# Optimization experiments

Hardware: AMD Instinct MI355X
Metric: run time of the kernel (lower is better)

## Reference

```python
import jax, jax.numpy as jnp
import numpy as np

N_HEADS = 16
D_K = 64  # d_model / n_heads = 1024 / 16


def setup_inputs() -> dict:
    key = jax.random.key(0)
    ks = jax.random.split(key, 7)
    B, S, D = 4, 2048, 1024
    scale = 1.0 / np.sqrt(D)
    return {
        "Q": jax.random.normal(ks[0], (B, S, D), dtype=jnp.float32),
        "K": jax.random.normal(ks[1], (B, S, D), dtype=jnp.float32),
        "V": jax.random.normal(ks[2], (B, S, D), dtype=jnp.float32),
        # Linear weights stored as [in, out] so y = x @ W (bias=False in original).
        "WQ": jax.random.normal(ks[3], (D, D), dtype=jnp.float32) * scale,
        "WK": jax.random.normal(ks[4], (D, D), dtype=jnp.float32) * scale,
        "WV": jax.random.normal(ks[5], (D, D), dtype=jnp.float32) * scale,
        "Wfc": jax.random.normal(ks[6], (D, D), dtype=jnp.float32) * scale,
    }


def reference(Q, K, V, WQ, WK, WV, Wfc):
    B = Q.shape[0]
    # NOTE: the original uses a raw reshape [B, S, H*dk] -> [B, H, S, dk]
    # (NOT the usual view+transpose); row-major reshape reproduces it exactly.
    q = (Q @ WQ).reshape(B, N_HEADS, -1, D_K)  # [B, H, S, dk]
    k = (K @ WK).reshape(B, N_HEADS, -1, D_K)
    v = (V @ WV).reshape(B, N_HEADS, -1, D_K)
    scores = jnp.einsum("bhqd,bhkd->bhqk", q, k) / jnp.sqrt(jnp.asarray(D_K, q.dtype))
    attn = jax.nn.softmax(scores, axis=-1)
    ctx = jnp.einsum("bhqk,bhkd->bhqd", attn, v)  # [B, H, S, dk]
    ctx = jnp.transpose(ctx, (0, 2, 1, 3)).reshape(B, -1, N_HEADS * D_K)  # [B, S, D]
    return ctx @ Wfc
```

## Files before the change

kernel.cpp:

```cpp
#include <hip/hip_runtime.h>
#include <stdint.h>
#include <math.h>


typedef __attribute__((ext_vector_type(8))) short short8;
typedef __attribute__((ext_vector_type(4))) float f32x4;
typedef __attribute__((ext_vector_type(16))) float f32x16;
typedef __attribute__((ext_vector_type(2))) unsigned int u32x2;
typedef __attribute__((ext_vector_type(4))) unsigned int u32x4;
typedef __attribute__((ext_vector_type(8))) _Float16 half8;

__device__ __forceinline__ unsigned short bf16rne(float f) {
  unsigned int u = __builtin_bit_cast(unsigned int, f);
  unsigned int r = u + 0x7FFFu + ((u >> 16) & 1u);
  return (unsigned short)(r >> 16);
}

__device__ __forceinline__ void gld_lds16(const void* g, void* l) {
  typedef __attribute__((address_space(3))) unsigned int lds_u32;
  typedef const __attribute__((address_space(1))) unsigned int glb_u32;
  __builtin_amdgcn_global_load_lds((glb_u32*)(uintptr_t)g,
                                   (lds_u32*)(unsigned int)(uintptr_t)l,
                                   16, 0, 0);
}

__device__ __forceinline__ unsigned pkrtz(float a, float b) {
  auto h = __builtin_amdgcn_cvt_pkrtz(a, b);
  return __builtin_bit_cast(unsigned, h);
}

__global__ void convert_x_kernel(const float* __restrict__ Q,
                                 const float* __restrict__ K,
                                 const float* __restrict__ V,
                                 unsigned short* __restrict__ Xb) {
  const int z = blockIdx.y;
  const float* src = (z == 0) ? Q : (z == 1) ? K : V;
  const size_t i0 = ((size_t)blockIdx.x * 256 + threadIdx.x) * 8;
  const f32x4 a = *(const f32x4*)(src + i0);
  const f32x4 c = *(const f32x4*)(src + i0 + 4);
  u32x4 o;
  o[0] = (unsigned)bf16rne(a[0]) | ((unsigned)bf16rne(a[1]) << 16);
  o[1] = (unsigned)bf16rne(a[2]) | ((unsigned)bf16rne(a[3]) << 16);
  o[2] = (unsigned)bf16rne(c[0]) | ((unsigned)bf16rne(c[1]) << 16);
  o[3] = (unsigned)bf16rne(c[2]) | ((unsigned)bf16rne(c[3]) << 16);
  *(u32x4*)(Xb + (size_t)z * 8388608 + i0) = o;
}

__global__ void convert_w_kernel(const float* __restrict__ W0,
                                 const float* __restrict__ W1,
                                 const float* __restrict__ W2,
                                 const float* __restrict__ W3,
                                 unsigned short* __restrict__ Wt) {
  const int z = blockIdx.z;
  const float* W = (z == 0) ? W0 : (z == 1) ? W1 : (z == 2) ? W2 : W3;
  unsigned short* dst = Wt + (size_t)z * 1048576;
  __shared__ float tile[32][33];
  const int tx = threadIdx.x & 31, ty = threadIdx.x >> 5;
  const int k0 = blockIdx.x * 32, n0 = blockIdx.y * 32;
#pragma unroll
  for (int yy = 0; yy < 32; yy += 8)
    tile[ty + yy][tx] = W[(size_t)(k0 + ty + yy) * 1024 + n0 + tx];
  __syncthreads();
#pragma unroll
  for (int yy = 0; yy < 32; yy += 8)
    dst[(size_t)(n0 + ty + yy) * 1024 + k0 + tx] = bf16rne(tile[tx][ty + yy]);
}

__global__ __launch_bounds__(256, 2) void gemm_bt_kernel(
    const unsigned short* __restrict__ A, const unsigned short* __restrict__ Bt,
    unsigned short* __restrict__ Cbf, float* __restrict__ Cf32, float scaleZ0) {
  constexpr int K = 1024, N = 1024;
  const int z = blockIdx.z;
  const unsigned short* Ab = A + (size_t)z * 8192 * 1024;
  const unsigned short* Bb = Bt + (size_t)z * 1024 * 1024;
  const int tid = threadIdx.x;
  const int lane = tid & 63;
  const int w = tid >> 6;
  const int l15 = lane & 15, quad = lane >> 4;
  const int rowBase = blockIdx.x * 128;
  const int colBase = blockIdx.y * 128;
  const int wrow = (w >> 1) * 64;
  const int wcol = (w & 1) * 64;
  __shared__ __align__(16) unsigned short As[128 * 32];
  __shared__ __align__(16) unsigned short Bs[128 * 32];

  const f32x4 z4 = {0.0f, 0.0f, 0.0f, 0.0f};
  f32x4 acc[4][4];
#pragma unroll
  for (int i = 0; i < 4; i++)
#pragma unroll
    for (int j = 0; j < 4; j++) acc[i][j] = z4;

  const int s0 = tid, s1 = tid + 256;
  const int rA0 = s0 >> 2, cA0 = (s0 & 3) * 8;
  const int rA1 = s1 >> 2, cA1 = (s1 & 3) * 8;

  for (int k0 = 0; k0 < K; k0 += 32) {
    gld_lds16(Ab + (size_t)(rowBase + rA0) * K + k0 + cA0, (void*)(As + s0 * 8));
    gld_lds16(Ab + (size_t)(rowBase + rA1) * K + k0 + cA1, (void*)(As + s1 * 8));
    gld_lds16(Bb + (size_t)(colBase + rA0) * K + k0 + cA0, (void*)(Bs + s0 * 8));
    gld_lds16(Bb + (size_t)(colBase + rA1) * K + k0 + cA1, (void*)(Bs + s1 * 8));
    __syncthreads();
    short8 af[4], bfr[4];
#pragma unroll
    for (int i = 0; i < 4; i++)
      af[i] = *(const short8*)(As + (wrow + i * 16 + l15) * 32 + quad * 8);
#pragma unroll
    for (int j = 0; j < 4; j++)
      bfr[j] = *(const short8*)(Bs + (wcol + j * 16 + l15) * 32 + quad * 8);
#pragma unroll
    for (int i = 0; i < 4; i++)
#pragma unroll
      for (int j = 0; j < 4; j++)
        acc[i][j] =
            __builtin_amdgcn_mfma_f32_16x16x32_bf16(af[i], bfr[j], acc[i][j], 0, 0, 0);
    __syncthreads();
  }

  const float sc = (z == 0) ? scaleZ0 : 1.0f;
#pragma unroll
  for (int i = 0; i < 4; i++) {
#pragma unroll
    for (int j = 0; j < 4; j++) {
#pragma unroll
      for (int r = 0; r < 4; r++) {
        const int row = rowBase + wrow + i * 16 + quad * 4 + r;
        const int col = colBase + wcol + j * 16 + l15;
        const float v = acc[i][j][r] * sc;
        if (Cbf != nullptr) {
          Cbf[(size_t)z * 8192 * 1024 + (size_t)row * N + col] = bf16rne(v);
        } else {
          Cf32[(size_t)row * N + col] = v;
        }
      }
    }
  }
}

__global__ void vtrans_kernel(const unsigned short* __restrict__ linv,
                              unsigned short* __restrict__ Vt) {
  const int st = blockIdx.x, bh = blockIdx.y;
  const unsigned short* vp = linv + (size_t)bh * 131072;
  __shared__ unsigned short tile[64 * 136];
  const int tid = threadIdx.x;
#pragma unroll
  for (int it = 0; it < 4; it++) {
    const int idx = it * 256 + tid;
    const int s = idx >> 3, d0 = (idx & 7) * 8;
    const u32x4 vv = *(const u32x4*)(vp + (size_t)(st * 128 + s) * 64 + d0);
#pragma unroll
    for (int m = 0; m < 4; m++) {
      const unsigned lo = vv[m] & 0xffffu, hi = vv[m] >> 16;
      const float f0 = __builtin_bit_cast(float, lo << 16);
      const float f1 = __builtin_bit_cast(float, hi << 16);
      const _Float16 h0 = (_Float16)f0, h1 = (_Float16)f1;
      tile[(d0 + 2 * m) * 136 + s] = __builtin_bit_cast(unsigned short, h0);
      tile[(d0 + 2 * m + 1) * 136 + s] = __builtin_bit_cast(unsigned short, h1);
    }
  }
  __syncthreads();
#pragma unroll
  for (int it = 0; it < 4; it++) {
    const int idx = it * 256 + tid;
    const int d = idx >> 4, s0 = (idx & 15) * 8;
    const u32x4 o = *(const u32x4*)(tile + d * 136 + s0);
    *(u32x4*)(Vt + (size_t)bh * 131072 + (size_t)d * 2048 + st * 128 + s0) = o;
  }
}

__global__ __launch_bounds__(256, 3) void attn_kernel(
    const unsigned short* __restrict__ lin, const _Float16* __restrict__ Vt,
    unsigned short* __restrict__ ctxr) {
  const int bh = blockIdx.x;
  const int qt = blockIdx.y;
  const int b = bh >> 4, h = bh & 15;
  const int tid = threadIdx.x, lane = tid & 63, w = tid >> 6;
  const int l31 = lane & 31, hl = lane >> 5, x7 = l31 & 7;
  const size_t headOff = (size_t)(b * 2048 + h * 128) * 1024;
  const unsigned short* qp = lin + headOff;
  const unsigned short* kp = lin + 8388608 + headOff;
  const _Float16* vtp = Vt + (size_t)bh * 131072;

  __shared__ __align__(16) unsigned short smem[24576];
  unsigned short(*Ks)[4096] = (unsigned short(*)[4096])smem;
  _Float16(*Vs)[4096] = (_Float16(*)[4096])(smem + 8192);
  _Float16* Pl = (_Float16*)(smem + 16384) + w * 2048;

  const int stageV = (w >= 2);
  const int wbase = (stageV ? (w - 2) : w) * 256 + lane;
  auto stage = [&](int bufn, int key0) {
#pragma unroll
    for (int i = 0; i < 4; i++) {
      const int slot = wbase + i * 64;
      const int row = slot >> 3;
      const int seg = (slot & 7) ^ (row & 7);
      if (!stageV) {
        gld_lds16(kp + (size_t)(key0 + row) * 64 + seg * 8,
                  (void*)(&Ks[bufn][slot * 8]));
      } else {
        gld_lds16(vtp + (size_t)row * 2048 + key0 + seg * 8,
                  (void*)(&Vs[bufn][slot * 8]));
      }
    }
  };

  const int qrow0 = qt * 128 + w * 32;
  short8 bq[4];
#pragma unroll
  for (int ks = 0; ks < 4; ks++)
    bq[ks] = *(const short8*)(qp + (size_t)(qrow0 + l31) * 64 + ks * 16 + hl * 8);

  f32x16 z16;
#pragma unroll
  for (int r = 0; r < 16; r++) z16[r] = 0.0f;
  f32x16 co[2] = {z16, z16};
  float mrun = -INFINITY, lrun = 0.0f;

  stage(0, 0);
  __syncthreads();

  for (int kt = 0; kt < 32; kt++) {
    const int cur = kt & 1;
    if (kt < 31) stage(cur ^ 1, (kt + 1) * 64);

    f32x16 sacc[2] = {z16, z16};
    __builtin_amdgcn_s_setprio(1);
#pragma unroll
    for (int g = 0; g < 2; g++) {
#pragma unroll
      for (int ks = 0; ks < 4; ks++) {
        const int slot = (g * 32 + l31) * 8 + ((2 * ks + hl) ^ x7);
        const short8 kf = *(const short8*)(&Ks[cur][slot * 8]);
        sacc[g] =
            __builtin_amdgcn_mfma_f32_32x32x16_bf16(kf, bq[ks], sacc[g], 0, 0, 0);
      }
    }
    __builtin_amdgcn_s_setprio(0);

    half8 vf[2][2][2];
#pragma unroll
    for (int dt = 0; dt < 2; dt++)
#pragma unroll
      for (int g = 0; g < 2; g++)
#pragma unroll
        for (int s = 0; s < 2; s++) {
          const int slot = (dt * 32 + l31) * 8 + ((4 * g + 2 * s + hl) ^ x7);
          vf[dt][g][s] = *(const half8*)(&Vs[cur][slot * 8]);
        }

    float pmax;
    {
      float tm[8];
#pragma unroll
      for (int r = 0; r < 8; r++)
        tm[r] = fmaxf(fmaxf(sacc[0][r], sacc[0][r + 8]),
                      fmaxf(sacc[1][r], sacc[1][r + 8]));
      const float a0 = fmaxf(fmaxf(tm[0], tm[1]), fmaxf(tm[2], tm[3]));
      const float a1 = fmaxf(fmaxf(tm[4], tm[5]), fmaxf(tm[6], tm[7]));
      pmax = fmaxf(a0, a1);
    }
    pmax = fmaxf(pmax, __shfl_xor(pmax, 32, 64));
    if (!__all(pmax - mrun <= 8.0f)) {
      const float mnew = fmaxf(mrun, pmax);
      const float a = exp2f(mrun - mnew);
      mrun = mnew;
      lrun *= a;
#pragma unroll
      for (int r = 0; r < 16; r++) {
        co[0][r] *= a;
        co[1][r] *= a;
      }
    }
    float ls0 = 0.0f, ls1 = 0.0f, ls2 = 0.0f, ls3 = 0.0f;
#pragma unroll
    for (int g = 0; g < 2; g++) {
#pragma unroll
      for (int r = 0; r < 16; r += 4) {
        const float p0 = exp2f(sacc[g][r + 0] - mrun);
        const float p1 = exp2f(sacc[g][r + 1] - mrun);
        const float p2 = exp2f(sacc[g][r + 2] - mrun);
        const float p3 = exp2f(sacc[g][r + 3] - mrun);
        sacc[g][r + 0] = p0;
        sacc[g][r + 1] = p1;
        sacc[g][r + 2] = p2;
        sacc[g][r + 3] = p3;
        ls0 += p0;
        ls1 += p1;
        ls2 += p2;
        ls3 += p3;
      }
    }
    lrun += (ls0 + ls1) + (ls2 + ls3);

#pragma unroll
    for (int g = 0; g < 2; g++) {
#pragma unroll
      for (int rg = 0; rg < 4; rg++) {
        u32x2 pw;
        pw[0] = pkrtz(sacc[g][4 * rg + 0], sacc[g][4 * rg + 1]);
        pw[1] = pkrtz(sacc[g][4 * rg + 2], sacc[g][4 * rg + 3]);
        *(u32x2*)(Pl + l31 * 64 + (((4 * g + rg) ^ x7) * 8) + hl * 4) = pw;
      }
      half8 pf[2];
#pragma unroll
      for (int s = 0; s < 2; s++)
        pf[s] =
            *(const half8*)(Pl + l31 * 64 + (((4 * g + 2 * s + hl) ^ x7) * 8));
      __builtin_amdgcn_s_setprio(1);
#pragma unroll
      for (int dt = 0; dt < 2; dt++)
#pragma unroll
        for (int s = 0; s < 2; s++)
          co[dt] = __builtin_amdgcn_mfma_f32_32x32x16_f16(vf[dt][g][s], pf[s],
                                                          co[dt], 0, 0, 0);
      __builtin_amdgcn_s_setprio(0);
    }
    __syncthreads();
  }

  lrun += __shfl_xor(lrun, 32, 64);
  const float inv = 1.0f / lrun;
  unsigned short* Cw = smem + w * 2304;
#pragma unroll
  for (int dt = 0; dt < 2; dt++) {
#pragma unroll
    for (int r = 0; r < 16; r++) {
      const int d = dt * 32 + (r & 3) + 8 * (r >> 2) + 4 * hl;
      Cw[l31 * 72 + d] = bf16rne(co[dt][r] * inv);
    }
  }
  __syncthreads();
#pragma unroll
  for (int it = 0; it < 4; it++) {
    const int q = it * 8 + (lane >> 3);
    const int seg = lane & 7;
    const u32x4 o = *(const u32x4*)(Cw + q * 72 + seg * 8);
    *(u32x4*)(ctxr + (size_t)(b * 2048 + qrow0 + q) * 1024 + h * 64 + seg * 8) = o;
  }
}

extern "C" void kernel_launch(void* const* d_in, const int* in_sizes, int n_in,
                              void* d_out, int out_size, void* d_ws, size_t ws_size,
                              hipStream_t stream) {
  const float* Q = (const float*)d_in[0];
  const float* K = (const float*)d_in[1];
  const float* V = (const float*)d_in[2];
  const float* WQ = (const float*)d_in[3];
  const float* WK = (const float*)d_in[4];
  const float* WV = (const float*)d_in[5];
  const float* Wfc = (const float*)d_in[6];
  float* out = (float*)d_out;

  unsigned short* ws = (unsigned short*)d_ws;
  unsigned short* Xb = ws;
  unsigned short* ctxr = ws;
  unsigned short* Vt = ws + 8388608;
  unsigned short* Wt = ws + 25165824;
  unsigned short* lin = ws + 29360128;

  convert_x_kernel<<<dim3(4096, 3), 256, 0, stream>>>(Q, K, V, Xb);
  convert_w_kernel<<<dim3(32, 32, 4), 256, 0, stream>>>(WQ, WK, WV, Wfc, Wt);
  const float qscale = 0.125f * 1.4426950408889634f;
  gemm_bt_kernel<<<dim3(64, 8, 3), 256, 0, stream>>>(Xb, Wt, lin, nullptr, qscale);
  vtrans_kernel<<<dim3(16, 64), 256, 0, stream>>>(lin + 16777216, Vt);
  attn_kernel<<<dim3(64, 16), 256, 0, stream>>>(lin, (const _Float16*)Vt, ctxr);
  gemm_bt_kernel<<<dim3(64, 8, 1), 256, 0, stream>>>(ctxr, Wt + 3 * 1048576, nullptr,
                                                     out, 1.0f);
}
```

Baseline: 422.5 us.

## Process two 32-row query groups per wave in attention to reuse K/V tiles

Each wave now handles 64 query rows (two groups of 32) instead of 32, so each block covers 256 queries and the grid's query dimension is halved. K and V fragments loaded from LDS are reused across both query groups, and the global-to-LDS staging of each K/V tile is amortized over twice as many queries. The cost is more registers per thread (doubled accumulators and softmax state), so launch bounds drop from 3 to 2 blocks per CU. The grid also shrinks to 512 blocks, which lowers parallelism.

```diff
diff --git a/kernel.cpp b/kernel.cpp
--- a/kernel.cpp
+++ b/kernel.cpp
@@ -168,7 +168,7 @@
   }
 }
 
-__global__ __launch_bounds__(256, 3) void attn_kernel(
+__global__ __launch_bounds__(256, 2) void attn_kernel(
     const unsigned short* __restrict__ lin, const _Float16* __restrict__ Vt,
     unsigned short* __restrict__ ctxr) {
   const int bh = blockIdx.x;
@@ -204,17 +204,22 @@
     }
   };
 
-  const int qrow0 = qt * 128 + w * 32;
-  short8 bq[4];
-#pragma unroll
-  for (int ks = 0; ks < 4; ks++)
-    bq[ks] = *(const short8*)(qp + (size_t)(qrow0 + l31) * 64 + ks * 16 + hl * 8);
+  const int qrow0 = qt * 256 + w * 64;
+  short8 bq[2][4];
+#pragma unroll
+  for (int qg = 0; qg < 2; qg++)
+#pragma unroll
+    for (int ks = 0; ks < 4; ks++)
+      bq[qg][ks] = *(const short8*)(qp +
+                                    (size_t)(qrow0 + qg * 32 + l31) * 64 +
+                                    ks * 16 + hl * 8);
 
   f32x16 z16;
 #pragma unroll
   for (int r = 0; r < 16; r++) z16[r] = 0.0f;
-  f32x16 co[2] = {z16, z16};
-  float mrun = -INFINITY, lrun = 0.0f;
+  f32x16 co[2][2] = {{z16, z16}, {z16, z16}};
+  float mrun[2] = {-INFINITY, -INFINITY};
+  float lrun[2] = {0.0f, 0.0f};
 
   stage(0, 0);
   __syncthreads();
@@ -223,18 +228,25 @@
     const int cur = kt & 1;
     if (kt < 31) stage(cur ^ 1, (kt + 1) * 64);
 
-    f32x16 sacc[2] = {z16, z16};
-    __builtin_amdgcn_s_setprio(1);
-#pragma unroll
-    for (int g = 0; g < 2; g++) {
+    short8 kf[2][4];
+#pragma unroll
+    for (int g = 0; g < 2; g++)
 #pragma unroll
       for (int ks = 0; ks < 4; ks++) {
         const int slot = (g * 32 + l31) * 8 + ((2 * ks + hl) ^ x7);
-        const short8 kf = *(const short8*)(&Ks[cur][slot * 8]);
-        sacc[g] =
-            __builtin_amdgcn_mfma_f32_32x32x16_bf16(kf, bq[ks], sacc[g], 0, 0, 0);
-      }
-    }
+        kf[g][ks] = *(const short8*)(&Ks[cur][slot * 8]);
+      }
+
+    f32x16 sacc[2][2] = {{z16, z16}, {z16, z16}};
+    __builtin_amdgcn_s_setprio(1);
+#pragma unroll
+    for (int qg = 0; qg < 2; qg++)
+#pragma unroll
+      for (int g = 0; g < 2; g++)
+#pragma unroll
+        for (int ks = 0; ks < 4; ks++)
+          sacc[qg][g] = __builtin_amdgcn_mfma_f32_32x32x16_bf16(
+              kf[g][ks], bq[qg][ks], sacc[qg][g], 0, 0, 0);
     __builtin_amdgcn_s_setprio(0);
 
     half8 vf[2][2][2];
@@ -248,90 +260,96 @@
           vf[dt][g][s] = *(const half8*)(&Vs[cur][slot * 8]);
         }
 
-    float pmax;
-    {
-      float tm[8];
-#pragma unroll
-      for (int r = 0; r < 8; r++)
-        tm[r] = fmaxf(fmaxf(sacc[0][r], sacc[0][r + 8]),
-                      fmaxf(sacc[1][r], sacc[1][r + 8]));
-      const float a0 = fmaxf(fmaxf(tm[0], tm[1]), fmaxf(tm[2], tm[3]));
-      const float a1 = fmaxf(fmaxf(tm[4], tm[5]), fmaxf(tm[6], tm[7]));
-      pmax = fmaxf(a0, a1);
-    }
-    pmax = fmaxf(pmax, __shfl_xor(pmax, 32, 64));
-    if (!__all(pmax - mrun <= 8.0f)) {
-      const float mnew = fmaxf(mrun, pmax);
-      const float a = exp2f(mrun - mnew);
-      mrun = mnew;
-      lrun *= a;
+#pragma unroll
+    for (int qg = 0; qg < 2; qg++) {
+      float pmax;
+      {
+        float tm[8];
+#pragma unroll
+        for (int r = 0; r < 8; r++)
+          tm[r] = fmaxf(fmaxf(sacc[qg][0][r], sacc[qg][0][r + 8]),
+                        fmaxf(sacc[qg][1][r], sacc[qg][1][r + 8]));
+        const float a0 = fmaxf(fmaxf(tm[0], tm[1]), fmaxf(tm[2], tm[3]));
+        const float a1 = fmaxf(fmaxf(tm[4], tm[5]), fmaxf(tm[6], tm[7]));
+        pmax = fmaxf(a0, a1);
+      }
+      pmax = fmaxf(pmax, __shfl_xor(pmax, 32, 64));
+      if (!__all(pmax - mrun[qg] <= 8.0f)) {
+        const float mnew = fmaxf(mrun[qg], pmax);
+        const float a = exp2f(mrun[qg] - mnew);
+        mrun[qg] = mnew;
+        lrun[qg] *= a;
+#pragma unroll
+        for (int r = 0; r < 16; r++) {
+          co[qg][0][r] *= a;
+          co[qg][1][r] *= a;
+        }
+      }
+      float ls0 = 0.0f, ls1 = 0.0f, ls2 = 0.0f, ls3 = 0.0f;
+#pragma unroll
+      for (int g = 0; g < 2; g++) {
+#pragma unroll
+        for (int r = 0; r < 16; r += 4) {
+          const float p0 = exp2f(sacc[qg][g][r + 0] - mrun[qg]);
+          const float p1 = exp2f(sacc[qg][g][r + 1] - mrun[qg]);
+          const float p2 = exp2f(sacc[qg][g][r + 2] - mrun[qg]);
+          const float p3 = exp2f(sacc[qg][g][r + 3] - mrun[qg]);
+          sacc[qg][g][r + 0] = p0;
+          sacc[qg][g][r + 1] = p1;
+          sacc[qg][g][r + 2] = p2;
+          sacc[qg][g][r + 3] = p3;
+          ls0 += p0;
+          ls1 += p1;
+          ls2 += p2;
+          ls3 += p3;
+        }
+      }
+      lrun[qg] += (ls0 + ls1) + (ls2 + ls3);
+
+#pragma unroll
+      for (int g = 0; g < 2; g++) {
+#pragma unroll
+        for (int rg = 0; rg < 4; rg++) {
+          u32x2 pw;
+          pw[0] = pkrtz(sacc[qg][g][4 * rg + 0], sacc[qg][g][4 * rg + 1]);
+          pw[1] = pkrtz(sacc[qg][g][4 * rg + 2], sacc[qg][g][4 * rg + 3]);
+          *(u32x2*)(Pl + l31 * 64 + (((4 * g + rg) ^ x7) * 8) + hl * 4) = pw;
+        }
+        half8 pf[2];
+#pragma unroll
+        for (int s = 0; s < 2; s++)
+          pf[s] =
+              *(const half8*)(Pl + l31 * 64 + (((4 * g + 2 * s + hl) ^ x7) * 8));
+        __builtin_amdgcn_s_setprio(1);
+#pragma unroll
+        for (int dt = 0; dt < 2; dt++)
+#pragma unroll
+          for (int s = 0; s < 2; s++)
+            co[qg][dt] = __builtin_amdgcn_mfma_f32_32x32x16_f16(
+                vf[dt][g][s], pf[s], co[qg][dt], 0, 0, 0);
+        __builtin_amdgcn_s_setprio(0);
+      }
+    }
+    __syncthreads();
+  }
+
+  unsigned short* Cw = smem + w * 4608;
+#pragma unroll
+  for (int qg = 0; qg < 2; qg++) {
+    const float l = lrun[qg] + __shfl_xor(lrun[qg], 32, 64);
+    const float inv = 1.0f / l;
+#pragma unroll
+    for (int dt = 0; dt < 2; dt++) {
 #pragma unroll
       for (int r = 0; r < 16; r++) {
-        co[0][r] *= a;
-        co[1][r] *= a;
-      }
-    }
-    float ls0 = 0.0f, ls1 = 0.0f, ls2 = 0.0f, ls3 = 0.0f;
-#pragma unroll
-    for (int g = 0; g < 2; g++) {
-#pragma unroll
-      for (int r = 0; r < 16; r += 4) {
-        const float p0 = exp2f(sacc[g][r + 0] - mrun);
-        const float p1 = exp2f(sacc[g][r + 1] - mrun);
-        const float p2 = exp2f(sacc[g][r + 2] - mrun);
-        const float p3 = exp2f(sacc[g][r + 3] - mrun);
-        sacc[g][r + 0] = p0;
-        sacc[g][r + 1] = p1;
-        sacc[g][r + 2] = p2;
-        sacc[g][r + 3] = p3;
-        ls0 += p0;
-        ls1 += p1;
-        ls2 += p2;
-        ls3 += p3;
-      }
-    }
-    lrun += (ls0 + ls1) + (ls2 + ls3);
-
-#pragma unroll
-    for (int g = 0; g < 2; g++) {
-#pragma unroll
-      for (int rg = 0; rg < 4; rg++) {
-        u32x2 pw;
-        pw[0] = pkrtz(sacc[g][4 * rg + 0], sacc[g][4 * rg + 1]);
-        pw[1] = pkrtz(sacc[g][4 * rg + 2], sacc[g][4 * rg + 3]);
-        *(u32x2*)(Pl + l31 * 64 + (((4 * g + rg) ^ x7) * 8) + hl * 4) = pw;
-      }
-      half8 pf[2];
-#pragma unroll
-      for (int s = 0; s < 2; s++)
-        pf[s] =
-            *(const half8*)(Pl + l31 * 64 + (((4 * g + 2 * s + hl) ^ x7) * 8));
-      __builtin_amdgcn_s_setprio(1);
-#pragma unroll
-      for (int dt = 0; dt < 2; dt++)
-#pragma unroll
-        for (int s = 0; s < 2; s++)
-          co[dt] = __builtin_amdgcn_mfma_f32_32x32x16_f16(vf[dt][g][s], pf[s],
-                                                          co[dt], 0, 0, 0);
-      __builtin_amdgcn_s_setprio(0);
-    }
-    __syncthreads();
-  }
-
-  lrun += __shfl_xor(lrun, 32, 64);
-  const float inv = 1.0f / lrun;
-  unsigned short* Cw = smem + w * 2304;
-#pragma unroll
-  for (int dt = 0; dt < 2; dt++) {
-#pragma unroll
-    for (int r = 0; r < 16; r++) {
-      const int d = dt * 32 + (r & 3) + 8 * (r >> 2) + 4 * hl;
-      Cw[l31 * 72 + d] = bf16rne(co[dt][r] * inv);
+        const int d = dt * 32 + (r & 3) + 8 * (r >> 2) + 4 * hl;
+        Cw[(qg * 32 + l31) * 72 + d] = bf16rne(co[qg][dt][r] * inv);
+      }
     }
   }
   __syncthreads();
 #pragma unroll
-  for (int it = 0; it < 4; it++) {
+  for (int it = 0; it < 8; it++) {
     const int q = it * 8 + (lane >> 3);
     const int seg = lane & 7;
     const u32x4 o = *(const u32x4*)(Cw + q * 72 + seg * 8);
@@ -363,7 +381,7 @@
   const float qscale = 0.125f * 1.4426950408889634f;
   gemm_bt_kernel<<<dim3(64, 8, 3), 256, 0, stream>>>(Xb, Wt, lin, nullptr, qscale);
   vtrans_kernel<<<dim3(16, 64), 256, 0, stream>>>(lin + 16777216, Vt);
-  attn_kernel<<<dim3(64, 16), 256, 0, stream>>>(lin, (const _Float16*)Vt, ctxr);
+  attn_kernel<<<dim3(64, 8), 256, 0, stream>>>(lin, (const _Float16*)Vt, ctxr);
   gemm_bt_kernel<<<dim3(64, 8, 1), 256, 0, stream>>>(ctxr, Wt + 3 * 1048576, nullptr,
                                                      out, 1.0f);
 }
```

Result: faster. 378.9 us (-10.3%).
